# Performance work log

Measured on AMD Instinct MI355X. Metric: run time of the kernel, lower is better.

## Reference

```python
import jax, jax.numpy as jnp
import numpy as np

N, D, HW, FF, DD = 128, 256, 28, 2048, 64
NP_ = D * DD  # num_params = hidden_dim * dim_dynamic = 16384
NH_SELF, NH_ENC = 8, 4


def _conv(x, w, b, stride=1):
    y = jax.lax.conv_general_dilated(x, w, (stride, stride), ((1, 1), (1, 1)),
                                     dimension_numbers=('NCHW', 'OIHW', 'NCHW'))
    return y + b[None, :, None, None]


def _bn(x, g, b):
    # eval-mode BatchNorm2d with running_mean=0, running_var=1
    return x * g[None, :, None, None] + b[None, :, None, None]


def _ln(x, g, b, eps=1e-5):
    m = x.mean(-1, keepdims=True)
    v = ((x - m) ** 2).mean(-1, keepdims=True)
    return (x - m) / jnp.sqrt(v + eps) * g + b


def _mha(x, qkv_w, qkv_b, out_w, out_b, nh):
    # x: (S, B, D) seq-first, like torch MultiheadAttention
    S, B, Dm = x.shape
    dh = Dm // nh
    q, k, v = jnp.split(x @ qkv_w.T + qkv_b, 3, axis=-1)
    q = q.reshape(S, B, nh, dh) * (1.0 / np.sqrt(dh))
    k = k.reshape(S, B, nh, dh)
    v = v.reshape(S, B, nh, dh)
    a = jax.nn.softmax(jnp.einsum('sbhd,tbhd->bhst', q, k), axis=-1)
    o = jnp.einsum('bhst,tbhd->sbhd', a, v).reshape(S, B, Dm)
    return o @ out_w.T + out_b


def _up2(x):
    return jnp.repeat(jnp.repeat(x, 2, axis=2), 2, axis=3)


def _pe(max_len, d):
    pos = jnp.arange(max_len, dtype=jnp.float32)[:, None]
    div = jnp.exp(jnp.arange(0, d, 2, dtype=jnp.float32) * (-np.log(10000.0) / d))
    pe = jnp.zeros((max_len, d), jnp.float32)
    pe = pe.at[:, 0::2].set(jnp.sin(pos * div)).at[:, 1::2].set(jnp.cos(pos * div))
    return pe[:, None, :]  # (max_len, 1, d)


def _forward(roi_features, pro_features, enc_conv_w, enc_conv_b, enc_bn_g, enc_bn_b, attn_qkv_w, attn_qkv_b, attn_out_w, attn_out_b, norm1_g, norm1_b, norm2_g, norm2_b, norm3_g, norm3_b, dyn_w, dyn_b, dnorm1_g, dnorm1_b, dnorm2_g, dnorm2_b, lin1_w, lin1_b, lin2_w, lin2_b, te_qkv_w, te_qkv_b, te_out_w, te_out_b, te_ln1_g, te_ln1_b, te_ln2_g, te_ln2_b, te_ff1_w, te_ff1_b, te_ff2_w, te_ff2_b, rec_conv_w, rec_conv_b, rec_bn_g, rec_bn_b, detA_w, detA_b, det_bnA_g, det_bnA_b, detB_w, detB_b, det_final_w, det_final_b, det_final_bn_g, det_final_bn_b):
    n = roi_features.shape[0]
    h4 = HW // 4
    # ---- k_encoder: two stride-2 conv+BN+ReLU, 28->14->7 ----
    feats_pyr = []
    k = roi_features
    for i in range(2):
        k = jax.nn.relu(_bn(_conv(k, enc_conv_w[i], enc_conv_b[i], stride=2), enc_bn_g[i], enc_bn_b[i]))
        feats_pyr.append(k)
    k = k.reshape(n, D, h4 * h4).transpose(2, 0, 1)  # (49, N, D)
    # ---- self-attention over query tokens ----
    pro = pro_features.reshape(-1, pro_features.shape[-2], D).transpose(1, 0, 2)  # (nq, bs*nf, D)
    pro = _ln(pro + _mha(pro, attn_qkv_w, attn_qkv_b, attn_out_w, attn_out_b, NH_SELF), norm1_g, norm1_b)
    pro = pro.transpose(1, 0, 2).reshape(1, -1, D)  # (1, N, D)
    # ---- DynamicConv_v2 instance interaction ----
    feats = k.transpose(1, 0, 2)  # (N, 49, D)
    params = (pro @ dyn_w.T + dyn_b).transpose(1, 0, 2)  # (N, 1, 2*NP_)
    p1 = params[:, :, :NP_].reshape(-1, D, DD)   # (N, D, 64)
    p2 = params[:, :, NP_:].reshape(-1, DD, D)   # (N, 64, D)
    f = jax.nn.elu(_ln(jnp.einsum('nsc,ncd->nsd', feats, p1), dnorm1_g, dnorm1_b))
    f = jax.nn.elu(_ln(jnp.einsum('nsd,ndc->nsc', f, p2), dnorm2_g, dnorm2_b))  # (N, 49, D)
    pro = feats + f
    obj = _ln(pro, norm2_g, norm2_b)
    # ---- FFN (ELU activation) ----
    obj2 = jax.nn.elu(obj @ lin1_w.T + lin1_b) @ lin2_w.T + lin2_b
    obj = _ln(obj + obj2, norm3_g, norm3_b)
    # ---- pos encoding + 3-layer TransformerEncoder (post-norm, relu, nhead=4) ----
    obj = obj.transpose(1, 0, 2)  # (49, N, D)
    obj = obj + _pe(h4 * h4, D)
    for l in range(3):
        a = _mha(obj, te_qkv_w[l], te_qkv_b[l], te_out_w[l], te_out_b[l], NH_ENC)
        obj = _ln(obj + a, te_ln1_g[l], te_ln1_b[l])
        ff = jax.nn.relu(obj @ te_ff1_w[l].T + te_ff1_b[l]) @ te_ff2_w[l].T + te_ff2_b[l]
        obj = _ln(obj + ff, te_ln2_g[l], te_ln2_b[l])
    obj = obj.transpose(1, 2, 0).reshape(n, D, h4, h4)
    kmap = k.transpose(1, 2, 0).reshape(n, D, h4, h4)
    # ---- gated rec/det decoder pyramid ----
    k_rec = kmap * jax.nn.sigmoid(obj)
    k_rec = jax.nn.relu(_bn(_conv(_up2(k_rec), rec_conv_w[0], rec_conv_b[0]), rec_bn_g[0], rec_bn_b[0])) + feats_pyr[0]
    k_det = _conv(jax.nn.relu(_bn(_conv(_up2(obj), detA_w[0], detA_b[0]), det_bnA_g[0], det_bnA_b[0])), detB_w[0], detB_b[0]) + feats_pyr[0]
    k_rec = k_rec * jax.nn.sigmoid(k_det)
    k_rec = jax.nn.relu(_bn(_conv(_up2(k_rec), rec_conv_w[1], rec_conv_b[1]), rec_bn_g[1], rec_bn_b[1])) + roi_features
    k_det = _conv(jax.nn.relu(_bn(_conv(_up2(k_det), detA_w[1], detA_b[1]), det_bnA_g[1], det_bnA_b[1])), detB_w[1], detB_b[1]) + roi_features
    k_rec = k_rec * jax.nn.sigmoid(k_det)
    # final decoder_layer: Upsample to (28,28) is identity here, then conv+BN+ReLU
    k_rec = jax.nn.relu(_bn(_conv(k_rec, det_final_w, det_final_b), det_final_bn_g, det_final_bn_b))
    return k_rec.reshape(n, D, HW * HW).transpose(0, 2, 1)  # (N, 784, D)


def setup_inputs():
    keys = iter(jax.random.split(jax.random.key(0), 80))
    def rn(shape, s=0.02):
        return jax.random.normal(next(keys), shape, jnp.float32) * s
    d = {
        'roi_features': jax.random.normal(next(keys), (N, D, HW, HW), jnp.float32),
        'pro_features': jax.random.normal(next(keys), (1, 1, N, D), jnp.float32),
        'gt_masks': jax.random.normal(next(keys), (N, HW, HW), jnp.float32),
        'enc_conv_w': rn((2, D, D, 3, 3)), 'enc_conv_b': rn((2, D)),
        'enc_bn_g': jnp.ones((2, D)), 'enc_bn_b': jnp.zeros((2, D)),
        'attn_qkv_w': rn((3 * D, D)), 'attn_qkv_b': rn((3 * D,)),
        'attn_out_w': rn((D, D)), 'attn_out_b': rn((D,)),
        'norm1_g': jnp.ones((D,)), 'norm1_b': jnp.zeros((D,)),
        'norm2_g': jnp.ones((D,)), 'norm2_b': jnp.zeros((D,)),
        'norm3_g': jnp.ones((D,)), 'norm3_b': jnp.zeros((D,)),
        'dyn_w': rn((2 * NP_, D)), 'dyn_b': rn((2 * NP_,)),
        'dnorm1_g': jnp.ones((DD,)), 'dnorm1_b': jnp.zeros((DD,)),
        'dnorm2_g': jnp.ones((D,)), 'dnorm2_b': jnp.zeros((D,)),
        'lin1_w': rn((FF, D)), 'lin1_b': rn((FF,)),
        'lin2_w': rn((D, FF)), 'lin2_b': rn((D,)),
        'te_qkv_w': rn((3, 3 * D, D)), 'te_qkv_b': rn((3, 3 * D)),
        'te_out_w': rn((3, D, D)), 'te_out_b': rn((3, D)),
        'te_ln1_g': jnp.ones((3, D)), 'te_ln1_b': jnp.zeros((3, D)),
        'te_ln2_g': jnp.ones((3, D)), 'te_ln2_b': jnp.zeros((3, D)),
        'te_ff1_w': rn((3, FF, D)), 'te_ff1_b': rn((3, FF)),
        'te_ff2_w': rn((3, D, FF)), 'te_ff2_b': rn((3, D)),
        'rec_conv_w': rn((2, D, D, 3, 3)), 'rec_conv_b': rn((2, D)),
        'rec_bn_g': jnp.ones((2, D)), 'rec_bn_b': jnp.zeros((2, D)),
        'detA_w': rn((2, D, D, 3, 3)), 'detA_b': rn((2, D)),
        'det_bnA_g': jnp.ones((2, D)), 'det_bnA_b': jnp.zeros((2, D)),
        'detB_w': rn((2, D, D, 3, 3)), 'detB_b': rn((2, D)),
        'det_final_w': rn((D, D, 3, 3)), 'det_final_b': rn((D,)),
        'det_final_bn_g': jnp.ones((D,)), 'det_final_bn_b': jnp.zeros((D,)),
    }
    return d


def reference(roi_features, pro_features, gt_masks, enc_conv_w, enc_conv_b, enc_bn_g, enc_bn_b, attn_qkv_w, attn_qkv_b, attn_out_w, attn_out_b, norm1_g, norm1_b, norm2_g, norm2_b, norm3_g, norm3_b, dyn_w, dyn_b, dnorm1_g, dnorm1_b, dnorm2_g, dnorm2_b, lin1_w, lin1_b, lin2_w, lin2_b, te_qkv_w, te_qkv_b, te_out_w, te_out_b, te_ln1_g, te_ln1_b, te_ln2_g, te_ln2_b, te_ff1_w, te_ff1_b, te_ff2_w, te_ff2_b, rec_conv_w, rec_conv_b, rec_bn_g, rec_bn_b, detA_w, detA_b, det_bnA_g, det_bnA_b, detB_w, detB_b, det_final_w, det_final_b, det_final_bn_g, det_final_bn_b):
    # gt_masks is only consumed by the (truncated) SequencePredictor head; unused here
    return _forward(roi_features, pro_features, enc_conv_w, enc_conv_b, enc_bn_g, enc_bn_b, attn_qkv_w, attn_qkv_b, attn_out_w, attn_out_b, norm1_g, norm1_b, norm2_g, norm2_b, norm3_g, norm3_b, dyn_w, dyn_b, dnorm1_g, dnorm1_b, dnorm2_g, dnorm2_b, lin1_w, lin1_b, lin2_w, lin2_b, te_qkv_w, te_qkv_b, te_out_w, te_out_b, te_ln1_g, te_ln1_b, te_ln2_g, te_ln2_b, te_ff1_w, te_ff1_b, te_ff2_w, te_ff2_b, rec_conv_w, rec_conv_b, rec_bn_g, rec_bn_b, detA_w, detA_b, det_bnA_g, det_bnA_b, detB_w, detB_b, det_final_w, det_final_b, det_final_bn_g, det_final_bn_b)
```

## Files before the change

kernel.cpp:

```cpp
#include <hip/hip_runtime.h>
#include <hip/hip_bf16.h>
#include <string.h>

typedef __hip_bfloat16 bf16;
typedef short bf16x8 __attribute__((ext_vector_type(8)));
typedef float f32x16 __attribute__((ext_vector_type(16)));

typedef __attribute__((address_space(3))) unsigned int       as3_u32;
typedef const __attribute__((address_space(1))) unsigned int as1_u32c;

__device__ __forceinline__ void dma16(const void* g, void* l){
  __builtin_amdgcn_global_load_lds((as1_u32c*)g, (as3_u32*)l, 16, 0, 0);
}

__device__ __align__(256) unsigned char g_zpad[256];

__device__ __forceinline__ float b2f(bf16 v){ return __bfloat162float(v); }
__device__ __forceinline__ bf16  f2b(float v){ return __float2bfloat16(v); }
__device__ __forceinline__ unsigned short f2bu(float v){
  union { bf16 b; unsigned short u; } x; x.b = __float2bfloat16(v); return x.u;
}
__device__ __forceinline__ float ldf(const float* p, size_t i){ return p[i]; }
__device__ __forceinline__ float ldf(const bf16*  p, size_t i){ return b2f(p[i]); }

__device__ __forceinline__ int xcd_swizzle(int lin, int nwg){
  int q = nwg >> 3, r = nwg & 7;
  int x = lin & 7, i = lin >> 3;
  int base = (x < r) ? x * (q + 1) : r * (q + 1) + (x - r) * q;
  return base + i;
}

__device__ __forceinline__ float2 block_stats256(float x, float* sred){
  float v = x;
  #pragma unroll
  for (int o = 32; o; o >>= 1) v += __shfl_xor(v, o);
  int w = threadIdx.x >> 6;
  if ((threadIdx.x & 63) == 0) sred[w] = v;
  __syncthreads();
  float mean = (sred[0] + sred[1] + sred[2] + sred[3]) * (1.f/256.f);
  __syncthreads();
  float d = x - mean;
  v = d * d;
  #pragma unroll
  for (int o = 32; o; o >>= 1) v += __shfl_xor(v, o);
  if ((threadIdx.x & 63) == 0) sred[w] = v;
  __syncthreads();
  float var = (sred[0] + sred[1] + sred[2] + sred[3]) * (1.f/256.f);
  __syncthreads();
  return make_float2(mean, var);
}

__global__ __launch_bounds__(256) void probe_k(const bf16* __restrict__ buf,
                                               unsigned long long len, float* score){
  __shared__ float sred[4];
  unsigned long long stride = len / 256ull; if (!stride) stride = 1;
  unsigned long long i = (unsigned long long)threadIdx.x * stride;
  if (i >= len) i = len - 1;
  float v = fabsf(b2f(buf[i]));
  #pragma unroll
  for (int o = 32; o; o >>= 1) v = fmaxf(v, __shfl_xor(v, o));
  if ((threadIdx.x & 63) == 0) sred[threadIdx.x >> 6] = v;
  __syncthreads();
  if (threadIdx.x == 0)
    score[0] = fmaxf(fmaxf(sred[0], sred[1]), fmaxf(sred[2], sred[3]));
}

__global__ void verdict_k(const float* score, int nstage, float* out){
  if (threadIdx.x == 0 && blockIdx.x == 0){
    for (int i = 0; i < nstage; i++){
      float s = score[i];
      if (!(s > 1e-8f)){
        float sent = 1000.f + 40.f * i;
        for (int j = 0; j < 64; j++) out[j] = sent;
        return;
      }
    }
  }
}

__global__ __launch_bounds__(256) void cvt_k(const float* __restrict__ s,
                                             bf16* __restrict__ d, int n4){
  int i = blockIdx.x * 256 + threadIdx.x;
  if (i < n4){
    float4 f = reinterpret_cast<const float4*>(s)[i];
    ushort4 u;
    u.x = f2bu(f.x); u.y = f2bu(f.y); u.z = f2bu(f.z); u.w = f2bu(f.w);
    reinterpret_cast<ushort4*>(d)[i] = u;
  }
}

__global__ __launch_bounds__(256) void troi_k(const float* __restrict__ roi,
                                              bf16* __restrict__ o){
  __shared__ float tile[64][65];
  int n = blockIdx.z, c0 = blockIdx.y * 64, p0 = blockIdx.x * 64;
  int a = threadIdx.x & 63, bq = threadIdx.x >> 6;
  #pragma unroll
  for (int cs = bq; cs < 64; cs += 4){
    int p = p0 + a;
    tile[cs][a] = (p < 784) ? roi[((size_t)n*256 + c0 + cs)*784 + p] : 0.f;
  }
  __syncthreads();
  #pragma unroll
  for (int ps = bq; ps < 64; ps += 4){
    int p = p0 + ps;
    if (p < 784) o[((size_t)n*784 + p)*256 + c0 + a] = f2b(tile[a][ps]);
  }
}

__global__ __launch_bounds__(256) void wtrans_k(const float* __restrict__ w,
                                                bf16* __restrict__ o){
  int co = blockIdx.x, t = threadIdx.x;
  const float* wp = w + (size_t)co * 2304 + (size_t)t * 9;
  #pragma unroll
  for (int tap = 0; tap < 9; tap++)
    o[(size_t)co * 2304 + tap * 256 + t] = f2b(wp[tap]);
}

__device__ __forceinline__ void mfma_step64(const unsigned short* As,
                                            const unsigned short* Bs,
                                            int wr, int wc, int lane,
                                            f32x16 (&acc)[2][2]){
  const char* asb = (const char*)As;
  const char* bsb = (const char*)Bs;
  int l31 = lane & 31;
  int lsw = (l31 & 7) << 4;
  int hi  = (lane >> 5) << 4;
  #pragma unroll
  for (int kb = 0; kb < 4; kb++){
    int cb = (kb*32 + hi) ^ lsw;
    bf16x8 a0 = *reinterpret_cast<const bf16x8*>(asb + (wr      + l31)*128 + cb);
    bf16x8 a1 = *reinterpret_cast<const bf16x8*>(asb + (wr + 32 + l31)*128 + cb);
    bf16x8 b0 = *reinterpret_cast<const bf16x8*>(bsb + (wc      + l31)*128 + cb);
    bf16x8 b1 = *reinterpret_cast<const bf16x8*>(bsb + (wc + 32 + l31)*128 + cb);
    acc[0][0] = __builtin_amdgcn_mfma_f32_32x32x16_bf16(a0, b0, acc[0][0], 0, 0, 0);
    acc[0][1] = __builtin_amdgcn_mfma_f32_32x32x16_bf16(a0, b1, acc[0][1], 0, 0, 0);
    acc[1][0] = __builtin_amdgcn_mfma_f32_32x32x16_bf16(a1, b0, acc[1][0], 0, 0, 0);
    acc[1][1] = __builtin_amdgcn_mfma_f32_32x32x16_bf16(a1, b1, acc[1][1], 0, 0, 0);
  }
}

template<int ACT>
__global__ __launch_bounds__(256) void gemm_mfma_k(
    const bf16* __restrict__ A, const bf16* __restrict__ W,
    const float* __restrict__ bias, bf16* __restrict__ C,
    int M, int N, int K)
{
  __shared__ __align__(16) unsigned short As[2][8192];
  __shared__ __align__(16) unsigned short Bs[2][8192];
  int t = threadIdx.x;
  int nbx = gridDim.x;
  int lin = blockIdx.y * nbx + blockIdx.x;
  int wg  = xcd_swizzle(lin, nbx * gridDim.y);
  int n0 = (wg % nbx) * 128, m0 = (wg / nbx) * 128;
  int lane = t & 63, wave = t >> 6;
  int wr = (wave >> 1) * 64, wc = (wave & 1) * 64;
  int lrow = lane >> 3;
  int e0   = (((lane & 7) ^ lrow) << 3);

  f32x16 acc[2][2];
  #pragma unroll
  for (int i = 0; i < 2; i++)
    #pragma unroll
    for (int j = 0; j < 2; j++)
      #pragma unroll
      for (int r = 0; r < 16; r++) acc[i][j][r] = 0.f;

  const bf16* apr[4]; const bf16* bpr[4];
  #pragma unroll
  for (int i = 0; i < 4; i++){
    int r = wave*32 + i*8 + lrow;
    apr[i] = A + (size_t)(m0 + r) * K + e0;
    bpr[i] = W + (size_t)(n0 + r) * K + e0;
  }

  auto stage = [&](int buf, int k0){
    #pragma unroll
    for (int i = 0; i < 4; i++){
      dma16(apr[i] + k0, &As[buf][(wave*32 + i*8) * 64]);
      dma16(bpr[i] + k0, &Bs[buf][(wave*32 + i*8) * 64]);
    }
  };

  int NIT = K >> 6;
  stage(0, 0);
  __syncthreads();
  #pragma unroll 1
  for (int it = 0; it < NIT; ++it){
    if (it + 1 < NIT) stage((it+1)&1, (it+1)*64);
    mfma_step64(As[it&1], Bs[it&1], wr, wc, lane, acc);
    __syncthreads();
  }

  int l31 = lane & 31;
  int rbase = m0 + wr + ((lane >> 5) << 2);
  #pragma unroll
  for (int j = 0; j < 2; j++){
    int n = n0 + wc + j*32 + l31;
    float bv = bias ? bias[n] : 0.f;
    #pragma unroll
    for (int i = 0; i < 2; i++){
      #pragma unroll
      for (int r = 0; r < 16; r++){
        int row = rbase + i*32 + (r & 3) + ((r >> 2) << 3);
        float v = acc[i][j][r] + bv;
        if (ACT == 1) v = fmaxf(v, 0.f);
        if (ACT == 2) v = v > 0.f ? v : (__expf(v) - 1.f);
        C[(size_t)row * N + n] = f2b(v);
      }
    }
  }
}

template<int Ho,int Wo,int Hi,int Wi,int UP2,int STRIDE,
         int HAS_BN,int RELU,int RES_MODE,int GATE,int WOUT,int OUTF>
__global__ __launch_bounds__(256) void conv_mfma_k(
    const bf16* __restrict__ in, const bf16* __restrict__ wTl,
    const float* __restrict__ cbias,
    const float* __restrict__ bng, const float* __restrict__ bnb,
    const void* __restrict__ res, bf16* __restrict__ gate,
    void* __restrict__ out)
{
  constexpr int HWo = Ho * Wo;
  constexpr int Hv = UP2 ? 2*Hi : Hi;
  constexpr int Wv = UP2 ? 2*Wi : Wi;
  __shared__ __align__(16) unsigned short As[2][8192];
  __shared__ __align__(16) unsigned short Bs[2][8192];
  int t = threadIdx.x;
  int nbx = gridDim.x;
  int lin = blockIdx.y * nbx + blockIdx.x;
  int wg  = xcd_swizzle(lin, nbx * gridDim.y);
  int co0 = (wg % nbx) * 128;
  int gp0 = (wg / nbx) * 128;
  int lane = t & 63, wave = t >> 6;
  int wr = (wave >> 1) * 64, wc = (wave & 1) * 64;
  int lrow = lane >> 3;
  int e0   = (((lane & 7) ^ lrow) << 3);

  int nA[4], oyA[4], oxA[4]; size_t wbase[4];
  #pragma unroll
  for (int i = 0; i < 4; i++){
    int r  = wave*32 + i*8 + lrow;
    int gp = gp0 + r;
    nA[i] = gp / HWo;
    int p = gp - nA[i] * HWo;
    oyA[i] = p / Wo; oxA[i] = p - oyA[i] * Wo;
    wbase[i] = (size_t)(co0 + r) * 2304;
  }

  f32x16 acc[2][2];
  #pragma unroll
  for (int i = 0; i < 2; i++)
    #pragma unroll
    for (int j = 0; j < 2; j++)
      #pragma unroll
      for (int r = 0; r < 16; r++) acc[i][j][r] = 0.f;

  auto stage = [&](int buf, int it){
    int tap = it >> 2, sub = it & 3;
    int ky = tap / 3, kx = tap - ky * 3;
    #pragma unroll
    for (int i = 0; i < 4; i++){
      int iy = oyA[i]*STRIDE + ky - 1;
      int ix = oxA[i]*STRIDE + kx - 1;
      bool val = (iy >= 0) && (iy < Hv) && (ix >= 0) && (ix < Wv);
      int sy = UP2 ? (iy >> 1) : iy;
      int sx = UP2 ? (ix >> 1) : ix;
      const bf16* sa = val
        ? in + (((size_t)nA[i] * Hi + sy) * Wi + sx) * 256 + sub*64 + e0
        : (const bf16*)g_zpad + e0;
      dma16(sa, &As[buf][(wave*32 + i*8) * 64]);
      const bf16* sb = wTl + wbase[i] + tap*256 + sub*64 + e0;
      dma16(sb, &Bs[buf][(wave*32 + i*8) * 64]);
    }
  };

  stage(0, 0);
  __syncthreads();
  #pragma unroll 1
  for (int it = 0; it < 36; ++it){
    if (it + 1 < 36) stage((it+1)&1, it+1);
    mfma_step64(As[it&1], Bs[it&1], wr, wc, lane, acc);
    __syncthreads();
  }

  int l31 = lane & 31;
  int rbase = gp0 + wr + ((lane >> 5) << 2);
  #pragma unroll
  for (int j = 0; j < 2; j++){
    int co = co0 + wc + j*32 + l31;
    float cb = cbias[co];
    float scale = 1.f, shift = cb;
    if (HAS_BN){ float g = bng[co]; scale = g; shift = cb*g + bnb[co]; }
    #pragma unroll
    for (int i = 0; i < 2; i++){
      #pragma unroll
      for (int r = 0; r < 16; r++){
        int grow = rbase + i*32 + (r & 3) + ((r >> 2) << 3);
        float v = acc[i][j][r] * scale + shift;
        if (RELU) v = fmaxf(v, 0.f);
        size_t oidx = (size_t)grow * 256 + co;
        if (RES_MODE == 1) v += b2f(((const bf16*)res)[oidx]);
        if (RES_MODE == 2){
          int rn = grow / HWo, rp = grow - rn * HWo;
          v += ((const float*)res)[((size_t)rn * 256 + co) * HWo + rp];
        }
        if (GATE){
          float gv = b2f(gate[oidx]);
          gate[oidx] = f2b(gv / (1.f + __expf(-v)));
        }
        if (WOUT){
          if (OUTF) ((float*)out)[oidx] = v;
          else      ((bf16*)out)[oidx]  = f2b(v);
        }
      }
    }
  }
}

template<int S, int NH, int DH>
__global__ __launch_bounds__(64) void attn_k(
    const bf16* __restrict__ qkv, bf16* __restrict__ out)
{
  const int D = NH * DH;
  int b = blockIdx.x / NH, h = blockIdx.x % NH;
  int chunk = blockIdx.y;
  int lane = threadIdx.x;
  __shared__ float ks[S][DH];
  __shared__ float vs[S][DH];
  __shared__ float os[64][DH];
  for (int idx = lane; idx < S*DH; idx += 64){
    int tt = idx / DH, d = idx % DH;
    size_t row = (size_t)(b*S + tt) * (3*D);
    ks[tt][d] = b2f(qkv[row +   D + h*DH + d]);
    vs[tt][d] = b2f(qkv[row + 2*D + h*DH + d]);
  }
  __syncthreads();
  int s = chunk*64 + lane;
  float q[DH];
  const float scale = 1.f / sqrtf((float)DH);
  if (s < S){
    size_t row = (size_t)(b*S + s) * (3*D);
    #pragma unroll
    for (int d = 0; d < DH; d++) q[d] = b2f(qkv[row + h*DH + d]) * scale;
  } else {
    #pragma unroll
    for (int d = 0; d < DH; d++) q[d] = 0.f;
  }
  float o[DH];
  #pragma unroll
  for (int d = 0; d < DH; d++) o[d] = 0.f;
  float m = -1e30f, l = 0.f;
  for (int tt = 0; tt < S; tt++){
    float sc = 0.f;
    #pragma unroll
    for (int d = 0; d < DH; d++) sc = fmaf(q[d], ks[tt][d], sc);
    float mn = fmaxf(m, sc);
    float corr = __expf(m - mn);
    float e = __expf(sc - mn);
    l = l * corr + e;
    #pragma unroll
    for (int d = 0; d < DH; d++) o[d] = fmaf(o[d], corr, e * vs[tt][d]);
    m = mn;
  }
  float inv = 1.f / l;
  #pragma unroll
  for (int d = 0; d < DH; d++) os[lane][d] = o[d] * inv;
  __syncthreads();
  for (int idx = lane; idx < 64*DH; idx += 64){
    int sl = idx / DH, d = idx % DH;
    int ss = chunk*64 + sl;
    if (ss < S) out[(size_t)(b*S + ss) * D + h*DH + d] = f2b(os[sl][d]);
  }
}

template<int ADD_PE, typename TA>
__global__ __launch_bounds__(256) void add_ln_k(
    const TA* __restrict__ a, const bf16* __restrict__ bsrc,
    const float* __restrict__ g, const float* __restrict__ bb, bf16* out)
{
  __shared__ float sred[4];
  int r = blockIdx.x, c = threadIdx.x;
  size_t idx = (size_t)r * 256 + c;
  float x = ldf(a, idx) + b2f(bsrc[idx]);
  float2 mv = block_stats256(x, sred);
  float y = (x - mv.x) * rsqrtf(mv.y + 1e-5f) * g[c] + bb[c];
  if (ADD_PE){
    int s = r % 49;
    float freq = __expf((float)(c & ~1) * (-9.210340371976184f / 256.f));
    float ang = (float)s * freq;
    y += (c & 1) ? cosf(ang) : sinf(ang);
  }
  out[idx] = f2b(y);
}

__global__ __launch_bounds__(256) void dyn_e1_k(
    const bf16* __restrict__ k2, const bf16* __restrict__ params,
    const float* __restrict__ g, const float* __restrict__ bb,
    bf16* __restrict__ f1)
{
  int n = blockIdx.x;
  int w = threadIdx.x >> 6, d = threadIdx.x & 63;
  const bf16* pp = params + (size_t)n * 32768 + d;
  for (int s = w; s < 49; s += 4){
    const bf16* fp = k2 + ((size_t)n*49 + s) * 256;
    float acc = 0.f;
    #pragma unroll 4
    for (int c = 0; c < 256; c++)
      acc = fmaf(b2f(fp[c]), b2f(pp[c*64]), acc);
    float v = acc;
    #pragma unroll
    for (int o = 32; o; o >>= 1) v += __shfl_xor(v, o);
    float mean = v * (1.f/64.f);
    float dd = acc - mean;
    v = dd * dd;
    #pragma unroll
    for (int o = 32; o; o >>= 1) v += __shfl_xor(v, o);
    float var = v * (1.f/64.f);
    float y = dd * rsqrtf(var + 1e-5f) * g[d] + bb[d];
    y = y > 0.f ? y : (__expf(y) - 1.f);
    f1[((size_t)n*49 + s) * 64 + d] = f2b(y);
  }
}

__global__ __launch_bounds__(256) void dyn_e2_k(
    const bf16* __restrict__ k2, const bf16* __restrict__ params,
    const bf16* __restrict__ f1,
    const float* __restrict__ g2, const float* __restrict__ bb2,
    const float* __restrict__ ng, const float* __restrict__ nb,
    bf16* __restrict__ obj0)
{
  __shared__ float sred[4];
  int ns = blockIdx.x; int n = ns / 49, s = ns % 49;
  int c = threadIdx.x;
  const bf16* pp  = params + (size_t)n * 32768 + 16384 + c;
  const bf16* f1p = f1 + (size_t)ns * 64;
  float acc = 0.f;
  #pragma unroll 8
  for (int d = 0; d < 64; d++)
    acc = fmaf(b2f(f1p[d]), b2f(pp[d*256]), acc);
  float2 mv = block_stats256(acc, sred);
  float y = (acc - mv.x) * rsqrtf(mv.y + 1e-5f) * g2[c] + bb2[c];
  y = y > 0.f ? y : (__expf(y) - 1.f);
  float pro2 = b2f(k2[((size_t)n*49 + s) * 256 + c]) + y;
  float2 mv2 = block_stats256(pro2, sred);
  float y2 = (pro2 - mv2.x) * rsqrtf(mv2.y + 1e-5f) * ng[c] + nb[c];
  obj0[(size_t)ns * 256 + c] = f2b(y2);
}

__global__ __launch_bounds__(256) void gate7_k(
    const bf16* __restrict__ k2, const bf16* __restrict__ obj,
    bf16* __restrict__ rec7)
{
  size_t idx = (size_t)blockIdx.x * 256 + threadIdx.x;
  float ov = b2f(obj[idx]);
  rec7[idx] = f2b(b2f(k2[idx]) / (1.f + __expf(-ov)));
}

extern "C" void kernel_launch(void* const* d_in, const int* in_sizes, int n_in,
                              void* d_out, int out_size, void* d_ws, size_t ws_size,
                              hipStream_t stream)
{
  (void)hipGetLastError();

  static float h_sent[64];
  auto send_sentinel = [&](float val){
    for (int i = 0; i < 64; i++) h_sent[i] = val;
    hipMemcpyAsync(d_out, h_sent, 256, hipMemcpyHostToDevice, stream);
  };

  static const int EXP_SIZES[53] = {
    25690112, 32768, 100352, 1179648, 512, 512, 512, 196608, 768, 65536,
    256, 256, 256, 256, 256, 256, 256, 8388608, 32768, 64,
    64, 256, 256, 524288, 2048, 524288, 256, 589824, 2304, 196608,
    768, 768, 768, 768, 768, 1572864, 6144, 1572864, 768, 1179648,
    512, 512, 512, 1179648, 512, 512, 512, 1179648, 512, 589824,
    256, 256, 256 };
  if (n_in != 53){ send_sentinel(6600.f + (float)n_in); return; }
  for (int i = 0; i < 53; i++)
    if (in_sizes[i] != EXP_SIZES[i]){ send_sentinel(6000.f + 10.f*i); return; }
  if (out_size != 25690112){ send_sentinel(3000.f + (float)(out_size >> 20)); return; }
  if (ws_size < 77070400ull){ send_sentinel(2000.f + (float)(ws_size >> 20)); return; }

  const float* roi    = (const float*)d_in[0];
  const float* proF   = (const float*)d_in[1];
  const float* encW   = (const float*)d_in[3];
  const float* encB   = (const float*)d_in[4];
  const float* encG   = (const float*)d_in[5];
  const float* encBB  = (const float*)d_in[6];
  const float* aqkvW  = (const float*)d_in[7];
  const float* aqkvB  = (const float*)d_in[8];
  const float* aoutW  = (const float*)d_in[9];
  const float* aoutB  = (const float*)d_in[10];
  const float* n1g    = (const float*)d_in[11];
  const float* n1b    = (const float*)d_in[12];
  const float* n2g    = (const float*)d_in[13];
  const float* n2b    = (const float*)d_in[14];
  const float* n3g    = (const float*)d_in[15];
  const float* n3b    = (const float*)d_in[16];
  const float* dynW   = (const float*)d_in[17];
  const float* dynB   = (const float*)d_in[18];
  const float* dn1g   = (const float*)d_in[19];
  const float* dn1b   = (const float*)d_in[20];
  const float* dn2g   = (const float*)d_in[21];
  const float* dn2b   = (const float*)d_in[22];
  const float* lin1W  = (const float*)d_in[23];
  const float* lin1B  = (const float*)d_in[24];
  const float* lin2W  = (const float*)d_in[25];
  const float* lin2B  = (const float*)d_in[26];
  const float* teqkvW = (const float*)d_in[27];
  const float* teqkvB = (const float*)d_in[28];
  const float* teoutW = (const float*)d_in[29];
  const float* teoutB = (const float*)d_in[30];
  const float* teln1g = (const float*)d_in[31];
  const float* teln1b = (const float*)d_in[32];
  const float* teln2g = (const float*)d_in[33];
  const float* teln2b = (const float*)d_in[34];
  const float* teff1W = (const float*)d_in[35];
  const float* teff1B = (const float*)d_in[36];
  const float* teff2W = (const float*)d_in[37];
  const float* teff2B = (const float*)d_in[38];
  const float* recW   = (const float*)d_in[39];
  const float* recB   = (const float*)d_in[40];
  const float* recG   = (const float*)d_in[41];
  const float* recBB  = (const float*)d_in[42];
  const float* dAW    = (const float*)d_in[43];
  const float* dAB    = (const float*)d_in[44];
  const float* dAG    = (const float*)d_in[45];
  const float* dABB   = (const float*)d_in[46];
  const float* dBW    = (const float*)d_in[47];
  const float* dBB_   = (const float*)d_in[48];
  const float* dfW    = (const float*)d_in[49];
  const float* dfB    = (const float*)d_in[50];
  const float* dfG    = (const float*)d_in[51];
  const float* dfBB   = (const float*)d_in[52];

  bf16* base   = (bf16*)d_ws;
  bf16* wT     = base + 0;
  bf16* k1     = base + 5308416;
  bf16* k2     = base + 11730944;
  bf16* qkvP   = base + 13336576;
  bf16* attoP  = base + 13434880;
  bf16* mhaP   = base + 13467648;
  bf16* proQ   = base + 13500416;
  bf16* f1     = base + 13533184;
  bf16* obj0   = base + 13934592;
  bf16* tmp    = base + 15540224;
  bf16* atto   = base + 17145856;
  bf16* obj    = base + 18751488;
  bf16* params = base + 20357120;
  bf16* rec7   = base + 20357120;
  bf16* hbuf   = base + 24551424;
  bf16* qkvT   = base + 24551424;
  bf16* C14    = base + 24551424;
  bf16* B14    = base + 32112640;
  bf16* B28    = base + 5308416;
  bf16* proB   = atto;
  bf16* roiT   = (bf16*)d_out;
  bf16* A14    = (bf16*)d_out;
  bf16* C28    = (bf16*)d_out + 6422528;
  bf16* gw     = (bf16*)d_out + 26214400;
  bf16* gqkvW  = gw + 0;
  bf16* gaoutW = gw + 196608;
  bf16* gdynW  = gw + 262144;
  bf16* glin1W = gw + 8650752;
  bf16* glin2W = gw + 9175040;
  bf16* gteqkvW= gw + 9699328;
  bf16* gteoutW= gw + 10289152;
  bf16* gteff1W= gw + 10485760;
  bf16* gteff2W= gw + 12058624;
  float* score = (float*)((char*)d_ws + 77070336);

  auto cvt = [&](const float* s, bf16* d, int n){
    cvt_k<<<(n/4 + 255)/256, 256, 0, stream>>>(s, d, n/4);
  };
  troi_k<<<dim3(13,4,128),256,0,stream>>>(roi, roiT);
  wtrans_k<<<256,256,0,stream>>>(encW,            wT + 0*589824);
  wtrans_k<<<256,256,0,stream>>>(encW + 589824,   wT + 1*589824);
  wtrans_k<<<256,256,0,stream>>>(recW,            wT + 2*589824);
  wtrans_k<<<256,256,0,stream>>>(recW + 589824,   wT + 3*589824);
  wtrans_k<<<256,256,0,stream>>>(dAW,             wT + 4*589824);
  wtrans_k<<<256,256,0,stream>>>(dAW + 589824,    wT + 5*589824);
  wtrans_k<<<256,256,0,stream>>>(dBW,             wT + 6*589824);
  wtrans_k<<<256,256,0,stream>>>(dBW + 589824,    wT + 7*589824);
  wtrans_k<<<256,256,0,stream>>>(dfW,             wT + 8*589824);
  cvt(proF,   proB,    32768);
  cvt(aqkvW,  gqkvW,   196608);
  cvt(aoutW,  gaoutW,  65536);
  cvt(dynW,   gdynW,   8388608);
  cvt(lin1W,  glin1W,  524288);
  cvt(lin2W,  glin2W,  524288);
  cvt(teqkvW, gteqkvW, 589824);
  cvt(teoutW, gteoutW, 196608);
  cvt(teff1W, gteff1W, 1572864);
  cvt(teff2W, gteff2W, 1572864);
  probe_k<<<1,256,0,stream>>>(roiT, 25690112ull, score+0);

  conv_mfma_k<14,14,28,28,0,2, 1,1,0,0,1,0><<<dim3(2,196),256,0,stream>>>(
      roiT, wT + 0*589824, encB, encG, encBB, nullptr, nullptr, k1);
  probe_k<<<1,256,0,stream>>>(k1, 6422528ull, score+1);
  conv_mfma_k<7,7,14,14,0,2, 1,1,0,0,1,0><<<dim3(2,49),256,0,stream>>>(
      k1, wT + 1*589824, encB+256, encG+256, encBB+256, nullptr, nullptr, k2);
  probe_k<<<1,256,0,stream>>>(k2, 1605632ull, score+2);

  gemm_mfma_k<0><<<dim3(6,1),256,0,stream>>>(proB, gqkvW, aqkvB, qkvP, 128,768,256);
  probe_k<<<1,256,0,stream>>>(qkvP, 98304ull, score+3);
  attn_k<128,8,32><<<dim3(8,2),64,0,stream>>>(qkvP, attoP);
  gemm_mfma_k<0><<<dim3(2,1),256,0,stream>>>(attoP, gaoutW, aoutB, mhaP, 128,256,256);
  add_ln_k<0,bf16><<<128,256,0,stream>>>(proB, mhaP, n1g, n1b, proQ);
  probe_k<<<1,256,0,stream>>>(proQ, 32768ull, score+4);

  gemm_mfma_k<0><<<dim3(256,1),256,0,stream>>>(proQ, gdynW, dynB, params, 128,32768,256);
  probe_k<<<1,256,0,stream>>>(params, 4194304ull, score+5);
  dyn_e1_k<<<128,256,0,stream>>>(k2, params, dn1g, dn1b, f1);
  probe_k<<<1,256,0,stream>>>(f1, 401408ull, score+6);
  dyn_e2_k<<<6272,256,0,stream>>>(k2, params, f1, dn2g, dn2b, n2g, n2b, obj0);
  probe_k<<<1,256,0,stream>>>(obj0, 1605632ull, score+7);

  gemm_mfma_k<2><<<dim3(16,49),256,0,stream>>>(obj0, glin1W, lin1B, hbuf, 6272,2048,256);
  gemm_mfma_k<0><<<dim3(2,49),256,0,stream>>>(hbuf, glin2W, lin2B, tmp, 6272,256,2048);
  add_ln_k<1,bf16><<<6272,256,0,stream>>>(obj0, tmp, n3g, n3b, obj);
  probe_k<<<1,256,0,stream>>>(obj, 1605632ull, score+8);

  for (int l = 0; l < 3; l++){
    gemm_mfma_k<0><<<dim3(6,49),256,0,stream>>>(
        obj, gteqkvW + (size_t)l*196608, teqkvB + l*768, qkvT, 6272,768,256);
    attn_k<49,4,64><<<dim3(512,1),64,0,stream>>>(qkvT, atto);
    gemm_mfma_k<0><<<dim3(2,49),256,0,stream>>>(
        atto, gteoutW + (size_t)l*65536, teoutB + l*256, tmp, 6272,256,256);
    add_ln_k<0,bf16><<<6272,256,0,stream>>>(obj, tmp, teln1g + l*256, teln1b + l*256, obj);
    gemm_mfma_k<1><<<dim3(16,49),256,0,stream>>>(
        obj, gteff1W + (size_t)l*524288, teff1B + l*2048, hbuf, 6272,2048,256);
    gemm_mfma_k<0><<<dim3(2,49),256,0,stream>>>(
        hbuf, gteff2W + (size_t)l*524288, teff2B + l*256, tmp, 6272,256,2048);
    add_ln_k<0,bf16><<<6272,256,0,stream>>>(obj, tmp, teln2g + l*256, teln2b + l*256, obj);
  }
  probe_k<<<1,256,0,stream>>>(obj, 1605632ull, score+9);

  gate7_k<<<6272,256,0,stream>>>(k2, obj, rec7);
  probe_k<<<1,256,0,stream>>>(rec7, 1605632ull, score+10);
  conv_mfma_k<14,14,7,7,1,1, 1,1,1,0,1,0><<<dim3(2,196),256,0,stream>>>(
      rec7, wT + 2*589824, recB, recG, recBB, k1, nullptr, B14);
  probe_k<<<1,256,0,stream>>>(B14, 6422528ull, score+11);
  conv_mfma_k<14,14,7,7,1,1, 1,1,0,0,1,0><<<dim3(2,196),256,0,stream>>>(
      obj, wT + 4*589824, dAB, dAG, dABB, nullptr, nullptr, C14);
  conv_mfma_k<14,14,14,14,0,1, 0,0,1,1,1,0><<<dim3(2,196),256,0,stream>>>(
      C14, wT + 6*589824, dBB_, nullptr, nullptr, k1, B14, A14);
  probe_k<<<1,256,0,stream>>>(A14, 6422528ull, score+12);
  conv_mfma_k<28,28,14,14,1,1, 1,1,2,0,1,0><<<dim3(2,784),256,0,stream>>>(
      B14, wT + 3*589824, recB+256, recG+256, recBB+256, roi, nullptr, B28);
  probe_k<<<1,256,0,stream>>>(B28, 25690112ull, score+13);
  conv_mfma_k<28,28,14,14,1,1, 1,1,0,0,1,0><<<dim3(2,784),256,0,stream>>>(
      A14, wT + 5*589824, dAB+256, dAG+256, dABB+256, nullptr, nullptr, C28);
  conv_mfma_k<28,28,28,28,0,1, 0,0,2,1,0,0><<<dim3(2,784),256,0,stream>>>(
      C28, wT + 7*589824, dBB_+256, nullptr, nullptr, roi, B28, nullptr);
  conv_mfma_k<28,28,28,28,0,1, 1,1,0,0,1,1><<<dim3(2,784),256,0,stream>>>(
      B28, wT + 8*589824, dfB, dfG, dfBB, nullptr, nullptr, d_out);

  verdict_k<<<1,64,0,stream>>>(score, 14, (float*)d_out);
  hipError_t le = hipGetLastError();
  if (le != hipSuccess){
    float v = 7000.f + 16.f * (float)(int)le;
    if (v > 60000.f) v = 60000.f;
    send_sentinel(v);
  }
}
```

Before: 2.454 ms.

## Drop LDS double buffering in GEMM and conv kernels for single-buffer staging

Replaces the double-buffered LDS staging in the GEMM and implicit-GEMM conv kernels with a single buffer. Each iteration now loads, syncs, computes, then syncs again. This halves LDS per block (64KB to 32KB), allowing more resident workgroups per CU. The conv kernel also computes per-tap address pointers once per tap instead of every sub-step, and the zero-pad buffer is enlarged so the sub-step offset stays in bounds. The cost is that global-to-LDS loads no longer overlap with MFMA compute within a block, so the design relies on occupancy to hide latency.

```diff
diff --git a/kernel.cpp b/kernel.cpp
--- a/kernel.cpp
+++ b/kernel.cpp
@@ -13,7 +13,7 @@
   __builtin_amdgcn_global_load_lds((as1_u32c*)g, (as3_u32*)l, 16, 0, 0);
 }
 
-__device__ __align__(256) unsigned char g_zpad[256];
+__device__ __align__(256) unsigned char g_zpad[1024];
 
 __device__ __forceinline__ float b2f(bf16 v){ return __bfloat162float(v); }
 __device__ __forceinline__ bf16  f2b(float v){ return __float2bfloat16(v); }
@@ -145,8 +145,8 @@
     const float* __restrict__ bias, bf16* __restrict__ C,
     int M, int N, int K)
 {
-  __shared__ __align__(16) unsigned short As[2][8192];
-  __shared__ __align__(16) unsigned short Bs[2][8192];
+  __shared__ __align__(16) unsigned short As[8192];
+  __shared__ __align__(16) unsigned short Bs[8192];
   int t = threadIdx.x;
   int nbx = gridDim.x;
   int lin = blockIdx.y * nbx + blockIdx.x;
@@ -173,21 +173,16 @@
     bpr[i] = W + (size_t)(n0 + r) * K + e0;
   }
 
-  auto stage = [&](int buf, int k0){
-    #pragma unroll
-    for (int i = 0; i < 4; i++){
-      dma16(apr[i] + k0, &As[buf][(wave*32 + i*8) * 64]);
-      dma16(bpr[i] + k0, &Bs[buf][(wave*32 + i*8) * 64]);
-    }
-  };
-
   int NIT = K >> 6;
-  stage(0, 0);
-  __syncthreads();
   #pragma unroll 1
   for (int it = 0; it < NIT; ++it){
-    if (it + 1 < NIT) stage((it+1)&1, (it+1)*64);
-    mfma_step64(As[it&1], Bs[it&1], wr, wc, lane, acc);
+    #pragma unroll
+    for (int i = 0; i < 4; i++){
+      dma16(apr[i] + it*64, &As[(wave*32 + i*8) * 64]);
+      dma16(bpr[i] + it*64, &Bs[(wave*32 + i*8) * 64]);
+    }
+    __syncthreads();
+    mfma_step64(As, Bs, wr, wc, lane, acc);
     __syncthreads();
   }
 
@@ -223,8 +218,8 @@
   constexpr int HWo = Ho * Wo;
   constexpr int Hv = UP2 ? 2*Hi : Hi;
   constexpr int Wv = UP2 ? 2*Wi : Wi;
-  __shared__ __align__(16) unsigned short As[2][8192];
-  __shared__ __align__(16) unsigned short Bs[2][8192];
+  __shared__ __align__(16) unsigned short As[8192];
+  __shared__ __align__(16) unsigned short Bs[8192];
   int t = threadIdx.x;
   int nbx = gridDim.x;
   int lin = blockIdx.y * nbx + blockIdx.x;
@@ -244,7 +239,7 @@
     nA[i] = gp / HWo;
     int p = gp - nA[i] * HWo;
     oyA[i] = p / Wo; oxA[i] = p - oyA[i] * Wo;
-    wbase[i] = (size_t)(co0 + r) * 2304;
+    wbase[i] = (size_t)(co0 + r) * 2304 + e0;
   }
 
   f32x16 acc[2][2];
@@ -255,31 +250,33 @@
       #pragma unroll
       for (int r = 0; r < 16; r++) acc[i][j][r] = 0.f;
 
-  auto stage = [&](int buf, int it){
-    int tap = it >> 2, sub = it & 3;
-    int ky = tap / 3, kx = tap - ky * 3;
-    #pragma unroll
-    for (int i = 0; i < 4; i++){
-      int iy = oyA[i]*STRIDE + ky - 1;
-      int ix = oxA[i]*STRIDE + kx - 1;
-      bool val = (iy >= 0) && (iy < Hv) && (ix >= 0) && (ix < Wv);
-      int sy = UP2 ? (iy >> 1) : iy;
-      int sx = UP2 ? (ix >> 1) : ix;
-      const bf16* sa = val
-        ? in + (((size_t)nA[i] * Hi + sy) * Wi + sx) * 256 + sub*64 + e0
-        : (const bf16*)g_zpad + e0;
-      dma16(sa, &As[buf][(wave*32 + i*8) * 64]);
-      const bf16* sb = wTl + wbase[i] + tap*256 + sub*64 + e0;
-      dma16(sb, &Bs[buf][(wave*32 + i*8) * 64]);
-    }
-  };
-
-  stage(0, 0);
-  __syncthreads();
+  const bf16* arp[4]; const bf16* brp[4];
+
   #pragma unroll 1
   for (int it = 0; it < 36; ++it){
-    if (it + 1 < 36) stage((it+1)&1, it+1);
-    mfma_step64(As[it&1], Bs[it&1], wr, wc, lane, acc);
+    int tap = it >> 2, sub = it & 3;
+    if (sub == 0){
+      int ky = tap / 3, kx = tap - ky * 3;
+      #pragma unroll
+      for (int i = 0; i < 4; i++){
+        int iy = oyA[i]*STRIDE + ky - 1;
+        int ix = oxA[i]*STRIDE + kx - 1;
+        bool val = (iy >= 0) && (iy < Hv) && (ix >= 0) && (ix < Wv);
+        int sy = UP2 ? (iy >> 1) : iy;
+        int sx = UP2 ? (ix >> 1) : ix;
+        arp[i] = val
+          ? in + (((size_t)nA[i] * Hi + sy) * Wi + sx) * 256 + e0
+          : (const bf16*)g_zpad + e0;
+        brp[i] = wTl + wbase[i] + tap*256;
+      }
+    }
+    #pragma unroll
+    for (int i = 0; i < 4; i++){
+      dma16(arp[i] + sub*64, &As[(wave*32 + i*8) * 64]);
+      dma16(brp[i] + sub*64, &Bs[(wave*32 + i*8) * 64]);
+    }
+    __syncthreads();
+    mfma_step64(As, Bs, wr, wc, lane, acc);
     __syncthreads();
   }
 
```

Measured after the change: 2.404 ms. -2.0%, faster.
